# Performance work log

Hardware: AMD Instinct MI355X
Metric: run time of the kernel (lower is better)

## Reference

```python
import jax, jax.numpy as jnp
import numpy as np

B, N, M, C, H = 256, 4096, 64, 512, 4
IN, OUT = 64, 64
EPS = 1e-8

def setup_inputs():
    key = jax.random.key(0)
    ks = jax.random.split(key, 8)
    def w(k, shape, scale=0.05):
        return jax.random.normal(k, shape, dtype=jnp.float32) * scale
    return {
        "in_data": jax.random.normal(ks[0], (B, IN), dtype=jnp.float32),
        "memory": jax.random.normal(ks[1], (B, N, M), dtype=jnp.float32),
        "h0": jnp.zeros((B, C), jnp.float32),
        "c0": jnp.zeros((B, C), jnp.float32),
        "prev_weights": jnp.zeros((2 * H, B, N), jnp.float32),
        "prev_reads": jax.random.normal(ks[2], (H, B, M), dtype=jnp.float32),
        "W_ih": w(ks[3], (4 * C, IN + H * M)),
        "b_ih": jnp.zeros((4 * C,), jnp.float32),
        "W_hh": w(ks[4], (4 * C, C)),
        "b_hh": jnp.zeros((4 * C,), jnp.float32),
        "W_out": w(ks[5], (OUT, C + H * M)),
        "b_out": jnp.zeros((OUT,), jnp.float32),
        "W_addr": w(ks[6], (2 * H, M + 6, C)),
        "b_addr": jnp.zeros((2 * H, M + 6), jnp.float32),
        "W_ea": w(ks[7], (H, 2 * M, C)),
        "b_ea": jnp.zeros((H, 2 * M), jnp.float32),
    }


def reference(in_data, memory, h0, c0, prev_weights, prev_reads,
              W_ih, b_ih, W_hh, b_hh, W_out, b_out,
              W_addr, b_addr, W_ea, b_ea):
    # ---- controller: LSTMCell over [input, prev_reads...] ----
    x = jnp.concatenate([in_data] + [prev_reads[i] for i in range(H)], axis=-1)  # [B, IN+H*M]
    gates = x @ W_ih.T + b_ih + h0 @ W_hh.T + b_hh                               # [B, 4C]
    i_g, f_g, g_g, o_g = jnp.split(gates, 4, axis=-1)
    c = jax.nn.sigmoid(f_g) * c0 + jax.nn.sigmoid(i_g) * jnp.tanh(g_g)
    h = jax.nn.sigmoid(o_g) * jnp.tanh(c)

    # ---- heads: alternate read / write, sequential over memory ----
    mem = memory
    reads = []
    for hi in range(2 * H):
        p = c @ W_addr[hi].T + b_addr[hi]                     # [B, M+6]
        k = jnp.tanh(p[:, :M])                                # key
        beta = jax.nn.softplus(p[:, M:M + 1])                 # key strength
        gate = jax.nn.sigmoid(p[:, M + 1:M + 2])              # interpolation gate
        s = jax.nn.softmax(p[:, M + 2:M + 5], axis=-1)        # shift weights (3)
        gamma = 1.0 + jax.nn.softplus(p[:, M + 5:M + 6])      # sharpening
        # content addressing: cosine similarity against all memory rows
        dot = jnp.einsum('bnm,bm->bn', mem, k)                # [B, N]
        norms = jnp.linalg.norm(mem, axis=-1) * jnp.linalg.norm(k, axis=-1, keepdims=True)
        wc = jax.nn.softmax(beta * dot / (norms + EPS), axis=-1)
        # interpolation with previous weights
        wg = gate * wc + (1.0 - gate) * prev_weights[hi]
        # circular shift convolution (shifts -1, 0, +1)
        ws = (s[:, 0:1] * jnp.roll(wg, 1, axis=-1)
              + s[:, 1:2] * wg
              + s[:, 2:3] * jnp.roll(wg, -1, axis=-1))
        # sharpening
        wp = ws ** gamma
        w = wp / (jnp.sum(wp, axis=-1, keepdims=True) + EPS)
        if hi % 2 == 0:  # read head
            reads.append(jnp.einsum('bn,bnm->bm', w, mem))
        else:            # write head: erase then add
            ea = c @ W_ea[hi // 2].T + b_ea[hi // 2]          # [B, 2M]
            e = jax.nn.sigmoid(ea[:, :M])
            a = jnp.tanh(ea[:, M:])
            mem = mem * (1.0 - w[:, :, None] * e[:, None, :]) + w[:, :, None] * a[:, None, :]

    # ---- output layer over [h, reads...] ----
    state = jnp.concatenate([h] + reads, axis=-1)             # [B, C+H*M]
    return jax.nn.sigmoid(state @ W_out.T + b_out)            # [B, OUT]
```

## Files before the change

### kernel.cpp

```cpp
#include <hip/hip_runtime.h>
#include <math.h>

#define EPSF 1e-8f
#define PLANE ((size_t)256 * 4096)

__device__ __forceinline__ float sigf(float x) { return 1.0f / (1.0f + expf(-x)); }
__device__ __forceinline__ float softplusf(float x) { return x > 20.0f ? x : log1pf(expf(x)); }
__device__ __forceinline__ float dot4(float4 a, float4 b) {
  return a.x * b.x + a.y * b.y + a.z * b.z + a.w * b.w;
}
__device__ __forceinline__ unsigned short f2bf(float x) {
  unsigned int u = __float_as_uint(x);
  unsigned int r = (u + 0x7FFF + ((u >> 16) & 1)) >> 16;
  return (unsigned short)r;
}
__device__ __forceinline__ float bf2f(unsigned int lo16) {
  return __uint_as_float(lo16 << 16);
}

__device__ __forceinline__ float gather_x(const float* __restrict__ in_data,
                                          const float* __restrict__ prev_reads,
                                          const float* __restrict__ h0,
                                          int row, int k) {
  if (k < 64) return in_data[row * 64 + k];
// ... 86 lines not shown
      acc[0][0] += a0 * w0; acc[0][1] += a0 * w1; acc[0][2] += a0 * w2; acc[0][3] += a0 * w3;
      acc[1][0] += a1 * w0; acc[1][1] += a1 * w1; acc[1][2] += a1 * w2; acc[1][3] += a1 * w3;
    }
    __syncthreads();
  }
  for (int i = 0; i < 2; i++)
    for (int j = 0; j < 4; j++) {
      int col = col0 + tx * 4 + j;
      if (col < 1072) {
        float bias = col < 560 ? b_addr[col] : b_ea[col - 560];
        p_raw[(size_t)(row0 + ty * 2 + i) * 1072 + col] = acc[i][j] + bias;
      }
    }
}

__global__ void head_params_kernel(const float* __restrict__ p_raw,
    float* __restrict__ kvec, float* __restrict__ knorm,
    float* __restrict__ betav, float* __restrict__ gatev,
    float* __restrict__ sv, float* __restrict__ gammav,
    float* __restrict__ evec, float* __restrict__ avec) {
  int hi = blockIdx.x, b = blockIdx.y, t = threadIdx.x;
  const float* p = p_raw + (size_t)b * 1072 + hi * 70;
  if (t < 64) {
    float kvv = tanhf(p[t]);
    kvec[((size_t)hi * 256 + b) * 64 + t] = kvv;
    float s = kvv * kvv;
    for (int m = 1; m < 64; m <<= 1) s += __shfl_xor(s, m);
    if (t == 0) {
      int hb = hi * 256 + b;
      knorm[hb] = sqrtf(s);
      betav[hb] = softplusf(p[64]);
      gatev[hb] = sigf(p[65]);
      float a0 = p[66], a1 = p[67], a2 = p[68];
      float mm = fmaxf(a0, fmaxf(a1, a2));
      float e0 = expf(a0 - mm), e1 = expf(a1 - mm), e2 = expf(a2 - mm);
      float es = e0 + e1 + e2;
      sv[hb * 3 + 0] = e0 / es; sv[hb * 3 + 1] = e1 / es; sv[hb * 3 + 2] = e2 / es;
      gammav[hb] = 1.0f + softplusf(p[69]);
    }
  } else if ((hi & 1) && hi < 7) {
    int wj = hi >> 1, t2 = t - 64;
    const float* ea = p_raw + (size_t)b * 1072 + 560 + wj * 128;
    evec[((size_t)wj * 256 + b) * 64 + t2] = sigf(ea[t2]);
    avec[((size_t)wj * 256 + b) * 64 + t2] = tanhf(ea[64 + t2]);
  }
}

__global__ void combo_kernel(const float* __restrict__ kvec,
                             const float* __restrict__ evec,
                             const float* __restrict__ avec,
                             float* __restrict__ combo, float* __restrict__ scal) {
  int b = blockIdx.x, m = threadIdx.x;
  size_t bm = (size_t)b * 64 + m;
  float k0 = kvec[0 * 16384 + bm], k1 = kvec[1 * 16384 + bm];
  float k2 = kvec[2 * 16384 + bm], k3 = kvec[3 * 16384 + bm];
  float k4 = kvec[4 * 16384 + bm], k5 = kvec[5 * 16384 + bm];
  float k6 = kvec[6 * 16384 + bm];
  float e1 = evec[0 * 16384 + bm], a1 = avec[0 * 16384 + bm];
  float e3 = evec[1 * 16384 + bm], a3 = avec[1 * 16384 + bm];
  float e5 = evec[2 * 16384 + bm], a5 = avec[2 * 16384 + bm];
  combo[0 * 16384 + bm] = k0;  combo[1 * 16384 + bm] = k1;
  combo[2 * 16384 + bm] = k2;  combo[3 * 16384 + bm] = e1 * k2;
  combo[4 * 16384 + bm] = k3;  combo[5 * 16384 + bm] = e1 * k3;
  combo[6 * 16384 + bm] = a1;  combo[7 * 16384 + bm] = e1 * a1;
  combo[8 * 16384 + bm] = e1;  combo[9 * 16384 + bm] = e1 * e1;
  combo[10 * 16384 + bm] = k4; combo[11 * 16384 + bm] = k5;
  combo[12 * 16384 + bm] = k6; combo[13 * 16384 + bm] = e5 * k6;
  combo[14 * 16384 + bm] = a5; combo[15 * 16384 + bm] = e5 * a5;
  combo[16 * 16384 + bm] = e5; combo[17 * 16384 + bm] = e5 * e5;
  combo[18 * 16384 + bm] = e3; combo[19 * 16384 + bm] = a3;
  float s0 = a1 * k2, s1 = a1 * k3, s2 = a1 * a1, s3 = a5 * k6, s4 = a5 * a5;
#pragma unroll
  for (int d = 1; d < 64; d <<= 1) {
    s0 += __shfl_xor(s0, d); s1 += __shfl_xor(s1, d); s2 += __shfl_xor(s2, d);
    s3 += __shfl_xor(s3, d); s4 += __shfl_xor(s4, d);
  }
  if (m == 0) {
    scal[b * 8 + 0] = s0; scal[b * 8 + 1] = s1; scal[b * 8 + 2] = s2;
    scal[b * 8 + 3] = s3; scal[b * 8 + 4] = s4;
  }
}

#define LDC(j, q) (*(const float4*)(cb + (size_t)(j) * 16384 + (q) * 4))

__global__ __launch_bounds__(256) void dotpass1_kernel(
    const float* __restrict__ mem, const float* __restrict__ combo,
    const float* __restrict__ knorm, const float* __restrict__ betav,
    const float* __restrict__ scal, float* __restrict__ P1,
    unsigned short* __restrict__ mem_bf) {
  extern __shared__ float4 tile[];
  const int NN = 4096;
  int b = blockIdx.y, n0 = blockIdx.x * 256, tid = threadIdx.x;
  const float4* m4 = (const float4*)mem + ((size_t)b * NN + n0) * 16;
  ushort4* mb4 = (ushort4*)mem_bf + ((size_t)b * NN + n0) * 16;
#pragma unroll
  for (int i = 0; i < 16; i++) {
    int L = tid + i * 256, r = L >> 4, q = L & 15;
    float4 v = m4[L];
    tile[r * 16 + (q ^ (r & 15))] = v;
    ushort4 o;
    o.x = f2bf(v.x); o.y = f2bf(v.y); o.z = f2bf(v.z); o.w = f2bf(v.w);
    mb4[L] = o;
  }
  __syncthreads();
  const float* cb = combo + (size_t)b * 64;
  float d0=0,d1=0,d2=0,d3=0,d4=0,d5=0,d6=0,d7=0,s0=0,s1=0,s2=0;
#pragma unroll
  for (int q = 0; q < 16; q++) {
    float4 v = tile[tid * 16 + (q ^ (tid & 15))];
    float4 sq = make_float4(v.x*v.x, v.y*v.y, v.z*v.z, v.w*v.w);
    d0 += dot4(v, LDC(0, q)); d1 += dot4(v, LDC(1, q));
    d2 += dot4(v, LDC(2, q)); d3 += dot4(v, LDC(3, q));
    d4 += dot4(v, LDC(4, q)); d5 += dot4(v, LDC(5, q));
    d6 += dot4(v, LDC(6, q)); d7 += dot4(v, LDC(7, q));
    s0 += sq.x + sq.y + sq.z + sq.w;
    s1 += dot4(sq, LDC(8, q)); s2 += dot4(sq, LDC(9, q));
  }
  float kn0 = knorm[0 * 256 + b], be0 = betav[0 * 256 + b];
  float kn1 = knorm[1 * 256 + b], be1 = betav[1 * 256 + b];
  float cak2 = scal[b * 8 + 0], cak3 = scal[b * 8 + 1], caa = scal[b * 8 + 2];
  float rn = sqrtf(s0);
  size_t o = (size_t)b * NN + n0 + tid;
  P1[0*PLANE+o] = be0 * d0 / (rn * kn0 + EPSF);
  P1[1*PLANE+o] = be1 * d1 / (rn * kn1 + EPSF);
  P1[2*PLANE+o] = d2; P1[3*PLANE+o] = d3 - cak2;
  P1[4*PLANE+o] = d4; P1[5*PLANE+o] = d5 - cak3;
  P1[6*PLANE+o] = s0; P1[7*PLANE+o] = s1 - d6; P1[8*PLANE+o] = s2 - 2.f*d7 + caa;
}

__global__ __launch_bounds__(256) void dotpass2_kernel(
    const unsigned short* __restrict__ mem_bf, const float* __restrict__ combo,
    const float* __restrict__ w_all, const float* __restrict__ knorm,
    const float* __restrict__ betav, const float* __restrict__ scal,
    float* __restrict__ P2) {
  __shared__ uint4 tileb[2048];
  const int NN = 4096;
  int b = blockIdx.y, n0 = blockIdx.x * 256, tid = threadIdx.x;
  size_t bo = (size_t)b * NN;
  const uint4* mb = (const uint4*)mem_bf + (bo + n0) * 8;
#pragma unroll
  for (int i = 0; i < 8; i++) {
    int G = tid + i * 256, r = G >> 3, g = G & 7;
    tileb[r * 8 + (g ^ (r & 7))] = mb[G];
  }
  __syncthreads();
  const float* cb = combo + (size_t)b * 64;
  float u1 = w_all[1 * PLANE + bo + n0 + tid];
  float u3 = w_all[3 * PLANE + bo + n0 + tid];
  float t0=0,t1=0,t2=0,t3=0,t4=0,t5=0,r0=0,r1=0,r2=0;
#pragma unroll
  for (int g = 0; g < 8; g++) {
    uint4 uv = tileb[tid * 8 + (g ^ (tid & 7))];
#pragma unroll
    for (int h = 0; h < 2; h++) {
      unsigned int pa = h ? uv.z : uv.x;
      unsigned int pb = h ? uv.w : uv.y;
      float4 v;
      v.x = bf2f(pa & 0xFFFFu); v.y = bf2f(pa >> 16);
      v.z = bf2f(pb & 0xFFFFu); v.w = bf2f(pb >> 16);
      int q = g * 2 + h;
      float4 e1 = LDC(8, q), aa1 = LDC(6, q), e3 = LDC(18, q), aa3 = LDC(19, q);
      float4 m1, m2;
      m1.x = v.x * (1.f - u1 * e1.x) + u1 * aa1.x;
      m1.y = v.y * (1.f - u1 * e1.y) + u1 * aa1.y;
      m1.z = v.z * (1.f - u1 * e1.z) + u1 * aa1.z;
      m1.w = v.w * (1.f - u1 * e1.w) + u1 * aa1.w;
      m2.x = m1.x * (1.f - u3 * e3.x) + u3 * aa3.x;
      m2.y = m1.y * (1.f - u3 * e3.y) + u3 * aa3.y;
      m2.z = m1.z * (1.f - u3 * e3.z) + u3 * aa3.z;
      m2.w = m1.w * (1.f - u3 * e3.w) + u3 * aa3.w;
      float4 sq = make_float4(m2.x*m2.x, m2.y*m2.y, m2.z*m2.z, m2.w*m2.w);
      t0 += dot4(m2, LDC(10, q)); t1 += dot4(m2, LDC(11, q));
      t2 += dot4(m2, LDC(12, q)); t3 += dot4(m2, LDC(13, q));
      t4 += dot4(m2, LDC(14, q)); t5 += dot4(m2, LDC(15, q));
      r0 += sq.x + sq.y + sq.z + sq.w;
      r1 += dot4(sq, LDC(16, q)); r2 += dot4(sq, LDC(17, q));
    }
  }
  float kn4 = knorm[4 * 256 + b], be4 = betav[4 * 256 + b];
  float kn5 = knorm[5 * 256 + b], be5 = betav[5 * 256 + b];
  float cak6 = scal[b * 8 + 3], caa6 = scal[b * 8 + 4];
  float rn = sqrtf(r0);
  size_t o = bo + n0 + tid;
  P2[0*PLANE+o] = be4 * t0 / (rn * kn4 + EPSF);
  P2[1*PLANE+o] = be5 * t1 / (rn * kn5 + EPSF);
  P2[2*PLANE+o] = t2; P2[3*PLANE+o] = t3 - cak6;
  P2[4*PLANE+o] = r0; P2[5*PLANE+o] = r1 - t4; P2[6*PLANE+o] = r2 - 2.f*t5 + caa6;
}

__global__ __launch_bounds__(256) void readpass_kernel(
    const unsigned short* __restrict__ mem_bf, const float* __restrict__ w_all,
    const float* __restrict__ evec, const float* __restrict__ avec,
    float* __restrict__ reads) {
  const int NN = 4096;
  int b = blockIdx.y, n0 = blockIdx.x * 256, tid = threadIdx.x;
  int wv = tid >> 6, lane = tid & 63, q = lane & 15, rl = lane >> 4;
  size_t bo = (size_t)b * NN;
  float4 e1 = *(const float4*)(evec + 0 * 16384 + b * 64 + q * 4);
  float4 a1 = *(const float4*)(avec + 0 * 16384 + b * 64 + q * 4);
  float4 e3 = *(const float4*)(evec + 1 * 16384 + b * 64 + q * 4);
  float4 a3 = *(const float4*)(avec + 1 * 16384 + b * 64 + q * 4);
  float4 e5 = *(const float4*)(evec + 2 * 16384 + b * 64 + q * 4);
  float4 a5 = *(const float4*)(avec + 2 * 16384 + b * 64 + q * 4);
  const float* w0r = w_all + 0 * PLANE + bo;
  const float* w1r = w_all + 1 * PLANE + bo;
  const float* w2r = w_all + 2 * PLANE + bo;
  const float* w3r = w_all + 3 * PLANE + bo;
  const float* w4r = w_all + 4 * PLANE + bo;
  const float* w5r = w_all + 5 * PLANE + bo;
  const float* w6r = w_all + 6 * PLANE + bo;
  __shared__ float sred[4][4][16][4];
  const ushort4* mb = (const ushort4*)mem_bf;
  float A[4][4] = {{0,0,0,0},{0,0,0,0},{0,0,0,0},{0,0,0,0}};
#pragma unroll 4
  for (int t = 0; t < 16; t++) {
    int nl = wv * 64 + t * 4 + rl, n = n0 + nl;
    ushort4 uv = mb[(bo + n0 + (size_t)nl) * 16 + q];
    float vx = bf2f(uv.x), vy = bf2f(uv.y), vz = bf2f(uv.z), vw = bf2f(uv.w);
    float w0v = w0r[n], u1 = w1r[n], w2v = w2r[n], u3 = w3r[n];
    float w4v = w4r[n], u5 = w5r[n], w6v = w6r[n];
    A[0][0] += w0v * vx; A[0][1] += w0v * vy; A[0][2] += w0v * vz; A[0][3] += w0v * vw;
    float m1x = vx * (1.f - u1 * e1.x) + u1 * a1.x;
    float m1y = vy * (1.f - u1 * e1.y) + u1 * a1.y;
    float m1z = vz * (1.f - u1 * e1.z) + u1 * a1.z;
    float m1w = vw * (1.f - u1 * e1.w) + u1 * a1.w;
    A[1][0] += w2v * m1x; A[1][1] += w2v * m1y; A[1][2] += w2v * m1z; A[1][3] += w2v * m1w;
    float m2x = m1x * (1.f - u3 * e3.x) + u3 * a3.x;
    float m2y = m1y * (1.f - u3 * e3.y) + u3 * a3.y;
    float m2z = m1z * (1.f - u3 * e3.z) + u3 * a3.z;
    float m2w = m1w * (1.f - u3 * e3.w) + u3 * a3.w;
    A[2][0] += w4v * m2x; A[2][1] += w4v * m2y; A[2][2] += w4v * m2z; A[2][3] += w4v * m2w;
    float m3x = m2x * (1.f - u5 * e5.x) + u5 * a5.x;
    float m3y = m2y * (1.f - u5 * e5.y) + u5 * a5.y;
    float m3z = m2z * (1.f - u5 * e5.z) + u5 * a5.z;
    float m3w = m2w * (1.f - u5 * e5.w) + u5 * a5.w;
    A[3][0] += w6v * m3x; A[3][1] += w6v * m3y; A[3][2] += w6v * m3z; A[3][3] += w6v * m3w;
  }
#pragma unroll
  for (int j = 0; j < 4; j++)
#pragma unroll
    for (int cmp = 0; cmp < 4; cmp++) {
      float x = A[j][cmp];
#pragma unroll
      for (int m = 16; m < 64; m <<= 1) x += __shfl_xor(x, m);
      A[j][cmp] = x;
    }
  if (rl == 0)
#pragma unroll
    for (int j = 0; j < 4; j++) {
      sred[j][wv][q][0] = A[j][0]; sred[j][wv][q][1] = A[j][1];
      sred[j][wv][q][2] = A[j][2]; sred[j][wv][q][3] = A[j][3];
    }
  __syncthreads();
  if (tid < 64) {
    int qq = tid >> 2, cc = tid & 3;
#pragma unroll
    for (int j = 0; j < 4; j++) {
      float s = sred[j][0][qq][cc] + sred[j][1][qq][cc] + sred[j][2][qq][cc] + sred[j][3][qq][cc];
      atomicAdd(&reads[j * 16384 + b * 64 + qq * 4 + cc], s);
    }
  }
}

template<int ND, int NE>
__global__ __launch_bounds__(256) void chain_kernel(
    const float* __restrict__ P, const float* __restrict__ uplane,
    const float* __restrict__ knorm, const float* __restrict__ betav,
    const float* __restrict__ gatev, const float* __restrict__ sv,
    const float* __restrict__ gammav, const float* __restrict__ prev_w,
    float* __restrict__ w_all, int head_base) {
  const int NN = 4096, BB = 256;
  int slot = blockIdx.x, b = blockIdx.y;
  int head = head_base + slot;
  size_t bo = (size_t)b * NN;
  __shared__ float wg[4096];
  __shared__ float redm[4], reds[4], reds2[4];
  int tid = threadIdx.x;
  int lane = tid & 63, wv = tid >> 6;
  int hb = head * BB + b;
  float kn = knorm[hb], be = betav[hb], ga = gatev[hb], gm = gammav[hb];
  float s0 = sv[hb * 3 + 0], s1 = sv[hb * 3 + 1], s2 = sv[hb * 3 + 2];
  const float* SC  = P + (size_t)slot * PLANE;
  const float* Da  = P + (size_t)(ND + 2 * (slot - ND)) * PLANE;
  const float* Dbc = Da + PLANE;
  const float* S0p = P + (size_t)(ND + 2 * NE) * PLANE;
  const float* T1p = S0p + PLANE;
  const float* T2p = T1p + PLANE;

  float sc[16];
  float mx = -1e30f;
#pragma unroll
  for (int i = 0; i < 16; i++) {
    int n = tid + i * 256;
    float scv;
    if (slot < ND) {
      scv = SC[bo + n];
    } else {
      float u = uplane[bo + n];
      float d = Da[bo + n] - u * Dbc[bo + n];
      float nn2 = S0p[bo + n] - 2.f * u * T1p[bo + n] + u * u * T2p[bo + n];
      nn2 = fmaxf(nn2, 0.f);
      scv = be * d / (sqrtf(nn2) * kn + EPSF);
    }
    sc[i] = scv;
    mx = fmaxf(mx, scv);
  }
  for (int m = 1; m < 64; m <<= 1) mx = fmaxf(mx, __shfl_xor(mx, m));
  if (lane == 0) redm[wv] = mx;
  __syncthreads();
  mx = fmaxf(fmaxf(redm[0], redm[1]), fmaxf(redm[2], redm[3]));
  float sum = 0.f;
#pragma unroll
  for (int i = 0; i < 16; i++) { sc[i] = expf(sc[i] - mx); sum += sc[i]; }
  for (int m = 1; m < 64; m <<= 1) sum += __shfl_xor(sum, m);
  if (lane == 0) reds[wv] = sum;
  __syncthreads();
  sum = reds[0] + reds[1] + reds[2] + reds[3];
  float inv = 1.0f / sum;
  const float* pw = prev_w + (size_t)head * BB * NN + bo;
#pragma unroll
  for (int i = 0; i < 16; i++) {
    int n = tid + i * 256;
    wg[n] = ga * (sc[i] * inv) + (1.f - ga) * pw[n];
  }
  __syncthreads();
  float wp[16];
  float sum2 = 0.f;
#pragma unroll
  for (int i = 0; i < 16; i++) {
    int n = tid + i * 256;
    float wsv = s0 * wg[(n + NN - 1) & (NN - 1)] + s1 * wg[n] + s2 * wg[(n + 1) & (NN - 1)];
    wp[i] = powf(wsv, gm);
    sum2 += wp[i];
  }
  for (int m = 1; m < 64; m <<= 1) sum2 += __shfl_xor(sum2, m);
  if (lane == 0) reds2[wv] = sum2;
  __syncthreads();
  sum2 = reds2[0] + reds2[1] + reds2[2] + reds2[3];
  float invs = 1.0f / (sum2 + EPSF);
  float* wo = w_all + (size_t)head * BB * NN + bo;
#pragma unroll
  for (int i = 0; i < 16; i++) wo[tid + i * 256] = wp[i] * invs;
}

__global__ __launch_bounds__(256) void gemm_out_kernel(
    const float* __restrict__ h, const float* __restrict__ reads,
    const float* __restrict__ W_out, const float* __restrict__ b_out,
    float* __restrict__ out) {
  __shared__ float As[16][33];
  __shared__ float Ws[16][65];
  int tid = threadIdx.x, tx = tid & 15, ty = tid >> 4;
  int row0 = blockIdx.y * 32;
  float acc[2][4] = {{0,0,0,0},{0,0,0,0}};
  for (int k0 = 0; k0 < 768; k0 += 16) {
    for (int i = tid; i < 32 * 16; i += 256) {
      int rr = i >> 4, cc = i & 15;
      int row = row0 + rr, k = k0 + cc;
// ... 41 lines not shown
  const float* b_out   = (const float*)d_in[11];
  const float* W_addr  = (const float*)d_in[12];
  const float* b_addr  = (const float*)d_in[13];
  const float* W_ea    = (const float*)d_in[14];
  const float* b_ea    = (const float*)d_in[15];
  float* out = (float*)d_out;
  (void)in_sizes; (void)n_in; (void)out_size; (void)ws_size;

  float* ws = (float*)d_ws;
  size_t off = 0;
  auto alloc = [&](size_t n) { float* p = ws + off; off += (n + 63) & ~(size_t)63; return p; };
  float* gates  = alloc(256 * 2048);
  float* cbuf   = alloc(256 * 512);
  float* hbuf   = alloc(256 * 512);
  float* p_raw  = alloc(256 * 1072);
  float* kvec   = alloc(8 * 256 * 64);
  float* knorm  = alloc(8 * 256);
  float* betav  = alloc(8 * 256);
  float* gatev  = alloc(8 * 256);
  float* sv     = alloc(8 * 256 * 3);
  float* gammav = alloc(8 * 256);
  float* evec   = alloc(3 * 256 * 64);
  float* avec   = alloc(3 * 256 * 64);
  float* combo  = alloc(20 * 256 * 64);
  float* scal   = alloc(256 * 8);
  float* P1     = alloc(9 * PLANE);
  float* P2     = alloc(7 * PLANE);
  float* w_all  = alloc(7 * PLANE);
  float* reads  = alloc(4 * 256 * 64);
  unsigned short* mem_bf = (unsigned short*)alloc(33554432);

  hipMemsetAsync(reads, 0, 4 * 256 * 64 * sizeof(float), stream);

  gemm_gates_kernel<<<dim3(32, 8), 256, 0, stream>>>(in_data, prev_r, h0, W_ih, W_hh, b_ih, b_hh, gates);
  lstm_elem_kernel<<<(256 * 512 + 255) / 256, 256, 0, stream>>>(gates, c0, cbuf, hbuf);
  gemm_heads_kernel<<<dim3(17, 8), 256, 0, stream>>>(cbuf, W_addr, W_ea, b_addr, b_ea, p_raw);
  head_params_kernel<<<dim3(8, 256), 128, 0, stream>>>(p_raw, kvec, knorm, betav, gatev, sv, gammav, evec, avec);
  combo_kernel<<<256, 64, 0, stream>>>(kvec, evec, avec, combo, scal);

  dim3 pgrid(16, 256);
  dotpass1_kernel<<<pgrid, 256, 65536, stream>>>(memory, combo, knorm, betav, scal, P1, mem_bf);
  chain_kernel<2, 2><<<dim3(4, 256), 256, 0, stream>>>(
      P1, w_all + 1 * PLANE, knorm, betav, gatev, sv, gammav, prev_w, w_all, 0);
  dotpass2_kernel<<<pgrid, 256, 0, stream>>>(mem_bf, combo, w_all, knorm, betav, scal, P2);
  chain_kernel<2, 1><<<dim3(3, 256), 256, 0, stream>>>(
      P2, w_all + 5 * PLANE, knorm, betav, gatev, sv, gammav, prev_w, w_all, 4);
  readpass_kernel<<<pgrid, 256, 0, stream>>>(mem_bf, w_all, evec, avec, reads);

  gemm_out_kernel<<<dim3(1, 8), 256, 0, stream>>>(hbuf, reads, W_out, b_out, out);
}
```

Measured before the change: 921.9 us.

## Fuse memory passes and chains into one per-batch mega kernel with fp16 planes

```diff
diff --git a/kernel.cpp b/kernel.cpp
--- a/kernel.cpp
+++ b/kernel.cpp
@@ -1,8 +1,11 @@
 #include <hip/hip_runtime.h>
+#include <hip/hip_fp16.h>
 #include <math.h>
 
 #define EPSF 1e-8f
-#define PLANE ((size_t)256 * 4096)
+#define NN 4096
+#define BB 256
+#define PH ((size_t)BB * NN)
 
 __device__ __forceinline__ float sigf(float x) { return 1.0f / (1.0f + expf(-x)); }
 __device__ __forceinline__ float softplusf(float x) { return x > 20.0f ? x : log1pf(expf(x)); }
@@ -124,62 +127,49 @@
     }
 }
 
-__global__ void head_params_kernel(const float* __restrict__ p_raw,
-    float* __restrict__ kvec, float* __restrict__ knorm,
-    float* __restrict__ betav, float* __restrict__ gatev,
-    float* __restrict__ sv, float* __restrict__ gammav,
-    float* __restrict__ evec, float* __restrict__ avec) {
-  int hi = blockIdx.x, b = blockIdx.y, t = threadIdx.x;
-  const float* p = p_raw + (size_t)b * 1072 + hi * 70;
-  if (t < 64) {
-    float kvv = tanhf(p[t]);
-    kvec[((size_t)hi * 256 + b) * 64 + t] = kvv;
-    float s = kvv * kvv;
-    for (int m = 1; m < 64; m <<= 1) s += __shfl_xor(s, m);
-    if (t == 0) {
-      int hb = hi * 256 + b;
+__global__ void params_kernel(const float* __restrict__ p_raw,
+    float* __restrict__ knorm, float* __restrict__ betav,
+    float* __restrict__ gatev, float* __restrict__ sv,
+    float* __restrict__ gammav, float* __restrict__ combo,
+    float* __restrict__ scal) {
+  int b = blockIdx.x, m = threadIdx.x;
+  const float* p = p_raw + (size_t)b * 1072;
+  float kv[7];
+#pragma unroll
+  for (int hi = 0; hi < 7; hi++) {
+    float k = tanhf(p[hi * 70 + m]);
+    kv[hi] = k;
+    float s = k * k;
+#pragma unroll
+    for (int d = 1; d < 64; d <<= 1) s += __shfl_xor(s, d);
+    if (m == 0) {
+      int hb = hi * BB + b;
       knorm[hb] = sqrtf(s);
-      betav[hb] = softplusf(p[64]);
-      gatev[hb] = sigf(p[65]);
-      float a0 = p[66], a1 = p[67], a2 = p[68];
+      betav[hb] = softplusf(p[hi * 70 + 64]);
+      gatev[hb] = sigf(p[hi * 70 + 65]);
+      float a0 = p[hi * 70 + 66], a1 = p[hi * 70 + 67], a2 = p[hi * 70 + 68];
       float mm = fmaxf(a0, fmaxf(a1, a2));
       float e0 = expf(a0 - mm), e1 = expf(a1 - mm), e2 = expf(a2 - mm);
       float es = e0 + e1 + e2;
       sv[hb * 3 + 0] = e0 / es; sv[hb * 3 + 1] = e1 / es; sv[hb * 3 + 2] = e2 / es;
-      gammav[hb] = 1.0f + softplusf(p[69]);
-    }
-  } else if ((hi & 1) && hi < 7) {
-    int wj = hi >> 1, t2 = t - 64;
-    const float* ea = p_raw + (size_t)b * 1072 + 560 + wj * 128;
-    evec[((size_t)wj * 256 + b) * 64 + t2] = sigf(ea[t2]);
-    avec[((size_t)wj * 256 + b) * 64 + t2] = tanhf(ea[64 + t2]);
-  }
-}
-
-__global__ void combo_kernel(const float* __restrict__ kvec,
-                             const float* __restrict__ evec,
-                             const float* __restrict__ avec,
-                             float* __restrict__ combo, float* __restrict__ scal) {
-  int b = blockIdx.x, m = threadIdx.x;
+      gammav[hb] = 1.0f + softplusf(p[hi * 70 + 69]);
+    }
+  }
+  float e1 = sigf(p[560 + 0 * 128 + m]),  a1v = tanhf(p[560 + 0 * 128 + 64 + m]);
+  float e3 = sigf(p[560 + 1 * 128 + m]),  a3v = tanhf(p[560 + 1 * 128 + 64 + m]);
+  float e5 = sigf(p[560 + 2 * 128 + m]),  a5v = tanhf(p[560 + 2 * 128 + 64 + m]);
   size_t bm = (size_t)b * 64 + m;
-  float k0 = kvec[0 * 16384 + bm], k1 = kvec[1 * 16384 + bm];
-  float k2 = kvec[2 * 16384 + bm], k3 = kvec[3 * 16384 + bm];
-  float k4 = kvec[4 * 16384 + bm], k5 = kvec[5 * 16384 + bm];
-  float k6 = kvec[6 * 16384 + bm];
-  float e1 = evec[0 * 16384 + bm], a1 = avec[0 * 16384 + bm];
-  float e3 = evec[1 * 16384 + bm], a3 = avec[1 * 16384 + bm];
-  float e5 = evec[2 * 16384 + bm], a5 = avec[2 * 16384 + bm];
-  combo[0 * 16384 + bm] = k0;  combo[1 * 16384 + bm] = k1;
-  combo[2 * 16384 + bm] = k2;  combo[3 * 16384 + bm] = e1 * k2;
-  combo[4 * 16384 + bm] = k3;  combo[5 * 16384 + bm] = e1 * k3;
-  combo[6 * 16384 + bm] = a1;  combo[7 * 16384 + bm] = e1 * a1;
-  combo[8 * 16384 + bm] = e1;  combo[9 * 16384 + bm] = e1 * e1;
-  combo[10 * 16384 + bm] = k4; combo[11 * 16384 + bm] = k5;
-  combo[12 * 16384 + bm] = k6; combo[13 * 16384 + bm] = e5 * k6;
-  combo[14 * 16384 + bm] = a5; combo[15 * 16384 + bm] = e5 * a5;
-  combo[16 * 16384 + bm] = e5; combo[17 * 16384 + bm] = e5 * e5;
-  combo[18 * 16384 + bm] = e3; combo[19 * 16384 + bm] = a3;
-  float s0 = a1 * k2, s1 = a1 * k3, s2 = a1 * a1, s3 = a5 * k6, s4 = a5 * a5;
+  combo[0 * 16384 + bm] = kv[0];  combo[1 * 16384 + bm] = kv[1];
+  combo[2 * 16384 + bm] = kv[2];  combo[3 * 16384 + bm] = e1 * kv[2];
+  combo[4 * 16384 + bm] = kv[3];  combo[5 * 16384 + bm] = e1 * kv[3];
+  combo[6 * 16384 + bm] = a1v;    combo[7 * 16384 + bm] = e1 * a1v;
+  combo[8 * 16384 + bm] = e1;     combo[9 * 16384 + bm] = e1 * e1;
+  combo[10 * 16384 + bm] = kv[4]; combo[11 * 16384 + bm] = kv[5];
+  combo[12 * 16384 + bm] = kv[6]; combo[13 * 16384 + bm] = e5 * kv[6];
+  combo[14 * 16384 + bm] = a5v;   combo[15 * 16384 + bm] = e5 * a5v;
+  combo[16 * 16384 + bm] = e5;    combo[17 * 16384 + bm] = e5 * e5;
+  combo[18 * 16384 + bm] = e3;    combo[19 * 16384 + bm] = a3v;
+  float s0 = a1v * kv[2], s1 = a1v * kv[3], s2 = a1v * a1v, s3 = a5v * kv[6], s4 = a5v * a5v;
 #pragma unroll
   for (int d = 1; d < 64; d <<= 1) {
     s0 += __shfl_xor(s0, d); s1 += __shfl_xor(s1, d); s2 += __shfl_xor(s2, d);
@@ -191,266 +181,323 @@
   }
 }
 
-#define LDC(j, q) (*(const float4*)(cb + (size_t)(j) * 16384 + (q) * 4))
-
-__global__ __launch_bounds__(256) void dotpass1_kernel(
-    const float* __restrict__ mem, const float* __restrict__ combo,
-    const float* __restrict__ knorm, const float* __restrict__ betav,
-    const float* __restrict__ scal, float* __restrict__ P1,
-    unsigned short* __restrict__ mem_bf) {
-  extern __shared__ float4 tile[];
-  const int NN = 4096;
-  int b = blockIdx.y, n0 = blockIdx.x * 256, tid = threadIdx.x;
-  const float4* m4 = (const float4*)mem + ((size_t)b * NN + n0) * 16;
-  ushort4* mb4 = (ushort4*)mem_bf + ((size_t)b * NN + n0) * 16;
-#pragma unroll
-  for (int i = 0; i < 16; i++) {
-    int L = tid + i * 256, r = L >> 4, q = L & 15;
-    float4 v = m4[L];
-    tile[r * 16 + (q ^ (r & 15))] = v;
-    ushort4 o;
-    o.x = f2bf(v.x); o.y = f2bf(v.y); o.z = f2bf(v.z); o.w = f2bf(v.w);
-    mb4[L] = o;
-  }
-  __syncthreads();
-  const float* cb = combo + (size_t)b * 64;
-  float d0=0,d1=0,d2=0,d3=0,d4=0,d5=0,d6=0,d7=0,s0=0,s1=0,s2=0;
-#pragma unroll
-  for (int q = 0; q < 16; q++) {
-    float4 v = tile[tid * 16 + (q ^ (tid & 15))];
-    float4 sq = make_float4(v.x*v.x, v.y*v.y, v.z*v.z, v.w*v.w);
-    d0 += dot4(v, LDC(0, q)); d1 += dot4(v, LDC(1, q));
-    d2 += dot4(v, LDC(2, q)); d3 += dot4(v, LDC(3, q));
-    d4 += dot4(v, LDC(4, q)); d5 += dot4(v, LDC(5, q));
-    d6 += dot4(v, LDC(6, q)); d7 += dot4(v, LDC(7, q));
-    s0 += sq.x + sq.y + sq.z + sq.w;
-    s1 += dot4(sq, LDC(8, q)); s2 += dot4(sq, LDC(9, q));
-  }
-  float kn0 = knorm[0 * 256 + b], be0 = betav[0 * 256 + b];
-  float kn1 = knorm[1 * 256 + b], be1 = betav[1 * 256 + b];
-  float cak2 = scal[b * 8 + 0], cak3 = scal[b * 8 + 1], caa = scal[b * 8 + 2];
-  float rn = sqrtf(s0);
-  size_t o = (size_t)b * NN + n0 + tid;
-  P1[0*PLANE+o] = be0 * d0 / (rn * kn0 + EPSF);
-  P1[1*PLANE+o] = be1 * d1 / (rn * kn1 + EPSF);
-  P1[2*PLANE+o] = d2; P1[3*PLANE+o] = d3 - cak2;
-  P1[4*PLANE+o] = d4; P1[5*PLANE+o] = d5 - cak3;
-  P1[6*PLANE+o] = s0; P1[7*PLANE+o] = s1 - d6; P1[8*PLANE+o] = s2 - 2.f*d7 + caa;
-}
-
-__global__ __launch_bounds__(256) void dotpass2_kernel(
-    const unsigned short* __restrict__ mem_bf, const float* __restrict__ combo,
-    const float* __restrict__ w_all, const float* __restrict__ knorm,
-    const float* __restrict__ betav, const float* __restrict__ scal,
-    float* __restrict__ P2) {
-  __shared__ uint4 tileb[2048];
-  const int NN = 4096;
-  int b = blockIdx.y, n0 = blockIdx.x * 256, tid = threadIdx.x;
-  size_t bo = (size_t)b * NN;
-  const uint4* mb = (const uint4*)mem_bf + (bo + n0) * 8;
-#pragma unroll
-  for (int i = 0; i < 8; i++) {
-    int G = tid + i * 256, r = G >> 3, g = G & 7;
-    tileb[r * 8 + (g ^ (r & 7))] = mb[G];
-  }
-  __syncthreads();
-  const float* cb = combo + (size_t)b * 64;
-  float u1 = w_all[1 * PLANE + bo + n0 + tid];
-  float u3 = w_all[3 * PLANE + bo + n0 + tid];
-  float t0=0,t1=0,t2=0,t3=0,t4=0,t5=0,r0=0,r1=0,r2=0;
-#pragma unroll
-  for (int g = 0; g < 8; g++) {
-    uint4 uv = tileb[tid * 8 + (g ^ (tid & 7))];
-#pragma unroll
-    for (int h = 0; h < 2; h++) {
-      unsigned int pa = h ? uv.z : uv.x;
-      unsigned int pb = h ? uv.w : uv.y;
-      float4 v;
-      v.x = bf2f(pa & 0xFFFFu); v.y = bf2f(pa >> 16);
-      v.z = bf2f(pb & 0xFFFFu); v.w = bf2f(pb >> 16);
-      int q = g * 2 + h;
-      float4 e1 = LDC(8, q), aa1 = LDC(6, q), e3 = LDC(18, q), aa3 = LDC(19, q);
-      float4 m1, m2;
-      m1.x = v.x * (1.f - u1 * e1.x) + u1 * aa1.x;
-      m1.y = v.y * (1.f - u1 * e1.y) + u1 * aa1.y;
-      m1.z = v.z * (1.f - u1 * e1.z) + u1 * aa1.z;
-      m1.w = v.w * (1.f - u1 * e1.w) + u1 * aa1.w;
-      m2.x = m1.x * (1.f - u3 * e3.x) + u3 * aa3.x;
-      m2.y = m1.y * (1.f - u3 * e3.y) + u3 * aa3.y;
-      m2.z = m1.z * (1.f - u3 * e3.z) + u3 * aa3.z;
-      m2.w = m1.w * (1.f - u3 * e3.w) + u3 * aa3.w;
-      float4 sq = make_float4(m2.x*m2.x, m2.y*m2.y, m2.z*m2.z, m2.w*m2.w);
-      t0 += dot4(m2, LDC(10, q)); t1 += dot4(m2, LDC(11, q));
-      t2 += dot4(m2, LDC(12, q)); t3 += dot4(m2, LDC(13, q));
-      t4 += dot4(m2, LDC(14, q)); t5 += dot4(m2, LDC(15, q));
-      r0 += sq.x + sq.y + sq.z + sq.w;
-      r1 += dot4(sq, LDC(16, q)); r2 += dot4(sq, LDC(17, q));
-    }
-  }
-  float kn4 = knorm[4 * 256 + b], be4 = betav[4 * 256 + b];
-  float kn5 = knorm[5 * 256 + b], be5 = betav[5 * 256 + b];
-  float cak6 = scal[b * 8 + 3], caa6 = scal[b * 8 + 4];
-  float rn = sqrtf(r0);
-  size_t o = bo + n0 + tid;
-  P2[0*PLANE+o] = be4 * t0 / (rn * kn4 + EPSF);
-  P2[1*PLANE+o] = be5 * t1 / (rn * kn5 + EPSF);
-  P2[2*PLANE+o] = t2; P2[3*PLANE+o] = t3 - cak6;
-  P2[4*PLANE+o] = r0; P2[5*PLANE+o] = r1 - t4; P2[6*PLANE+o] = r2 - 2.f*t5 + caa6;
-}
-
-__global__ __launch_bounds__(256) void readpass_kernel(
-    const unsigned short* __restrict__ mem_bf, const float* __restrict__ w_all,
-    const float* __restrict__ evec, const float* __restrict__ avec,
-    float* __restrict__ reads) {
-  const int NN = 4096;
-  int b = blockIdx.y, n0 = blockIdx.x * 256, tid = threadIdx.x;
-  int wv = tid >> 6, lane = tid & 63, q = lane & 15, rl = lane >> 4;
-  size_t bo = (size_t)b * NN;
-  float4 e1 = *(const float4*)(evec + 0 * 16384 + b * 64 + q * 4);
-  float4 a1 = *(const float4*)(avec + 0 * 16384 + b * 64 + q * 4);
-  float4 e3 = *(const float4*)(evec + 1 * 16384 + b * 64 + q * 4);
-  float4 a3 = *(const float4*)(avec + 1 * 16384 + b * 64 + q * 4);
-  float4 e5 = *(const float4*)(evec + 2 * 16384 + b * 64 + q * 4);
-  float4 a5 = *(const float4*)(avec + 2 * 16384 + b * 64 + q * 4);
-  const float* w0r = w_all + 0 * PLANE + bo;
-  const float* w1r = w_all + 1 * PLANE + bo;
-  const float* w2r = w_all + 2 * PLANE + bo;
-  const float* w3r = w_all + 3 * PLANE + bo;
-  const float* w4r = w_all + 4 * PLANE + bo;
-  const float* w5r = w_all + 5 * PLANE + bo;
-  const float* w6r = w_all + 6 * PLANE + bo;
-  __shared__ float sred[4][4][16][4];
-  const ushort4* mb = (const ushort4*)mem_bf;
-  float A[4][4] = {{0,0,0,0},{0,0,0,0},{0,0,0,0},{0,0,0,0}};
-#pragma unroll 4
-  for (int t = 0; t < 16; t++) {
-    int nl = wv * 64 + t * 4 + rl, n = n0 + nl;
-    ushort4 uv = mb[(bo + n0 + (size_t)nl) * 16 + q];
-    float vx = bf2f(uv.x), vy = bf2f(uv.y), vz = bf2f(uv.z), vw = bf2f(uv.w);
-    float w0v = w0r[n], u1 = w1r[n], w2v = w2r[n], u3 = w3r[n];
-    float w4v = w4r[n], u5 = w5r[n], w6v = w6r[n];
-    A[0][0] += w0v * vx; A[0][1] += w0v * vy; A[0][2] += w0v * vz; A[0][3] += w0v * vw;
-    float m1x = vx * (1.f - u1 * e1.x) + u1 * a1.x;
-    float m1y = vy * (1.f - u1 * e1.y) + u1 * a1.y;
-    float m1z = vz * (1.f - u1 * e1.z) + u1 * a1.z;
-    float m1w = vw * (1.f - u1 * e1.w) + u1 * a1.w;
-    A[1][0] += w2v * m1x; A[1][1] += w2v * m1y; A[1][2] += w2v * m1z; A[1][3] += w2v * m1w;
-    float m2x = m1x * (1.f - u3 * e3.x) + u3 * a3.x;
-    float m2y = m1y * (1.f - u3 * e3.y) + u3 * a3.y;
-    float m2z = m1z * (1.f - u3 * e3.z) + u3 * a3.z;
-    float m2w = m1w * (1.f - u3 * e3.w) + u3 * a3.w;
-    A[2][0] += w4v * m2x; A[2][1] += w4v * m2y; A[2][2] += w4v * m2z; A[2][3] += w4v * m2w;
-    float m3x = m2x * (1.f - u5 * e5.x) + u5 * a5.x;
-    float m3y = m2y * (1.f - u5 * e5.y) + u5 * a5.y;
-    float m3z = m2z * (1.f - u5 * e5.z) + u5 * a5.z;
-    float m3w = m2w * (1.f - u5 * e5.w) + u5 * a5.w;
-    A[3][0] += w6v * m3x; A[3][1] += w6v * m3y; A[3][2] += w6v * m3z; A[3][3] += w6v * m3w;
-  }
-#pragma unroll
-  for (int j = 0; j < 4; j++)
-#pragma unroll
-    for (int cmp = 0; cmp < 4; cmp++) {
-      float x = A[j][cmp];
-#pragma unroll
-      for (int m = 16; m < 64; m <<= 1) x += __shfl_xor(x, m);
-      A[j][cmp] = x;
-    }
-  if (rl == 0)
-#pragma unroll
-    for (int j = 0; j < 4; j++) {
-      sred[j][wv][q][0] = A[j][0]; sred[j][wv][q][1] = A[j][1];
-      sred[j][wv][q][2] = A[j][2]; sred[j][wv][q][3] = A[j][3];
-    }
-  __syncthreads();
-  if (tid < 64) {
-    int qq = tid >> 2, cc = tid & 3;
-#pragma unroll
-    for (int j = 0; j < 4; j++) {
-      float s = sred[j][0][qq][cc] + sred[j][1][qq][cc] + sred[j][2][qq][cc] + sred[j][3][qq][cc];
-      atomicAdd(&reads[j * 16384 + b * 64 + qq * 4 + cc], s);
-    }
-  }
-}
-
-template<int ND, int NE>
-__global__ __launch_bounds__(256) void chain_kernel(
-    const float* __restrict__ P, const float* __restrict__ uplane,
+#define CL(j, q) (*(const float4*)(cb + (j) * 64 + (q) * 4))
+
+__device__ void chain_dev(int tid, int b, int head,
+    const __half* __restrict__ SC, const __half* __restrict__ Da,
+    const __half* __restrict__ Dbc, const __half* __restrict__ S0p,
+    const __half* __restrict__ T1p, const __half* __restrict__ T2p,
+    const __half* w_h, int u_head, __half* w_out,
+    float* wg, float* red,
     const float* __restrict__ knorm, const float* __restrict__ betav,
     const float* __restrict__ gatev, const float* __restrict__ sv,
-    const float* __restrict__ gammav, const float* __restrict__ prev_w,
-    float* __restrict__ w_all, int head_base) {
-  const int NN = 4096, BB = 256;
-  int slot = blockIdx.x, b = blockIdx.y;
-  int head = head_base + slot;
-  size_t bo = (size_t)b * NN;
-  __shared__ float wg[4096];
-  __shared__ float redm[4], reds[4], reds2[4];
-  int tid = threadIdx.x;
+    const float* __restrict__ gammav, const float* __restrict__ prev_w) {
   int lane = tid & 63, wv = tid >> 6;
   int hb = head * BB + b;
   float kn = knorm[hb], be = betav[hb], ga = gatev[hb], gm = gammav[hb];
   float s0 = sv[hb * 3 + 0], s1 = sv[hb * 3 + 1], s2 = sv[hb * 3 + 2];
-  const float* SC  = P + (size_t)slot * PLANE;
-  const float* Da  = P + (size_t)(ND + 2 * (slot - ND)) * PLANE;
-  const float* Dbc = Da + PLANE;
-  const float* S0p = P + (size_t)(ND + 2 * NE) * PLANE;
-  const float* T1p = S0p + PLANE;
-  const float* T2p = T1p + PLANE;
-
-  float sc[16];
+  size_t bo = (size_t)b * NN;
+  const float* pw = prev_w + (size_t)head * PH + bo;
+  float sc[8];
   float mx = -1e30f;
 #pragma unroll
-  for (int i = 0; i < 16; i++) {
-    int n = tid + i * 256;
+  for (int i = 0; i < 8; i++) {
+    int n = tid + i * 512;
     float scv;
-    if (slot < ND) {
-      scv = SC[bo + n];
+    if (SC != nullptr) {
+      scv = __half2float(SC[bo + n]);
     } else {
-      float u = uplane[bo + n];
-      float d = Da[bo + n] - u * Dbc[bo + n];
-      float nn2 = S0p[bo + n] - 2.f * u * T1p[bo + n] + u * u * T2p[bo + n];
+      float u = __half2float(w_h[u_head * NN + n]);
+      float d = __half2float(Da[bo + n]) - u * __half2float(Dbc[bo + n]);
+      float nn2 = __half2float(S0p[bo + n]) - 2.f * u * __half2float(T1p[bo + n])
+                + u * u * __half2float(T2p[bo + n]);
       nn2 = fmaxf(nn2, 0.f);
       scv = be * d / (sqrtf(nn2) * kn + EPSF);
     }
-    sc[i] = scv;
-    mx = fmaxf(mx, scv);
-  }
+    sc[i] = scv; mx = fmaxf(mx, scv);
+  }
+#pragma unroll
   for (int m = 1; m < 64; m <<= 1) mx = fmaxf(mx, __shfl_xor(mx, m));
-  if (lane == 0) redm[wv] = mx;
+  if (lane == 0) red[wv] = mx;
   __syncthreads();
-  mx = fmaxf(fmaxf(redm[0], redm[1]), fmaxf(redm[2], redm[3]));
+  mx = red[0];
+#pragma unroll
+  for (int w = 1; w < 8; w++) mx = fmaxf(mx, red[w]);
   float sum = 0.f;
 #pragma unroll
-  for (int i = 0; i < 16; i++) { sc[i] = expf(sc[i] - mx); sum += sc[i]; }
+  for (int i = 0; i < 8; i++) { sc[i] = expf(sc[i] - mx); sum += sc[i]; }
+#pragma unroll
   for (int m = 1; m < 64; m <<= 1) sum += __shfl_xor(sum, m);
-  if (lane == 0) reds[wv] = sum;
+  if (lane == 0) red[8 + wv] = sum;
   __syncthreads();
-  sum = reds[0] + reds[1] + reds[2] + reds[3];
+  sum = 0.f;
+#pragma unroll
+  for (int w = 0; w < 8; w++) sum += red[8 + w];
   float inv = 1.0f / sum;
-  const float* pw = prev_w + (size_t)head * BB * NN + bo;
-#pragma unroll
-  for (int i = 0; i < 16; i++) {
-    int n = tid + i * 256;
+#pragma unroll
+  for (int i = 0; i < 8; i++) {
+    int n = tid + i * 512;
     wg[n] = ga * (sc[i] * inv) + (1.f - ga) * pw[n];
   }
   __syncthreads();
-  float wp[16];
+  float wp[8];
   float sum2 = 0.f;
 #pragma unroll
-  for (int i = 0; i < 16; i++) {
-    int n = tid + i * 256;
+  for (int i = 0; i < 8; i++) {
+    int n = tid + i * 512;
     float wsv = s0 * wg[(n + NN - 1) & (NN - 1)] + s1 * wg[n] + s2 * wg[(n + 1) & (NN - 1)];
     wp[i] = powf(wsv, gm);
     sum2 += wp[i];
   }
+#pragma unroll
   for (int m = 1; m < 64; m <<= 1) sum2 += __shfl_xor(sum2, m);
-  if (lane == 0) reds2[wv] = sum2;
+  if (lane == 0) red[16 + wv] = sum2;
   __syncthreads();
-  sum2 = reds2[0] + reds2[1] + reds2[2] + reds2[3];
+  sum2 = 0.f;
+#pragma unroll
+  for (int w = 0; w < 8; w++) sum2 += red[16 + w];
   float invs = 1.0f / (sum2 + EPSF);
-  float* wo = w_all + (size_t)head * BB * NN + bo;
-#pragma unroll
-  for (int i = 0; i < 16; i++) wo[tid + i * 256] = wp[i] * invs;
+#pragma unroll
+  for (int i = 0; i < 8; i++) {
+    int n = tid + i * 512;
+    w_out[n] = __float2half(wp[i] * invs);
+  }
+  __syncthreads();
+}
+
+__global__ __launch_bounds__(512, 2) void mega_kernel(
+    const float* __restrict__ mem, const float* __restrict__ combo,
+    const float* __restrict__ scal, const float* __restrict__ knorm,
+    const float* __restrict__ betav, const float* __restrict__ gatev,
+    const float* __restrict__ sv, const float* __restrict__ gammav,
+    const float* __restrict__ prev_w, unsigned short* __restrict__ mem_bf,
+    __half* __restrict__ P, float* __restrict__ reads) {
+  extern __shared__ char smem[];
+  __half* w_h   = (__half*)smem;
+  float*  cb    = (float*)(smem + 57344);
+  float*  scr   = (float*)(smem + 62464);
+  char*   un    = smem + 84992;
+  float4* tile32 = (float4*)un;
+  uint4*  tileb  = (uint4*)un;
+  float*  wg     = (float*)un;
+
+  int b = blockIdx.x, tid = threadIdx.x;
+  size_t bo = (size_t)b * NN;
+
+  for (int i = tid; i < 1280; i += 512) {
+    int j = i >> 6, m = i & 63;
+    cb[i] = combo[(size_t)j * 16384 + b * 64 + m];
+  }
+  __syncthreads();
+
+  {
+    float kn0 = knorm[0 * BB + b], be0 = betav[0 * BB + b];
+    float kn1 = knorm[1 * BB + b], be1 = betav[1 * BB + b];
+    float cak2 = scal[b * 8 + 0], cak3 = scal[b * 8 + 1], caa1 = scal[b * 8 + 2];
+    const float4* m4 = (const float4*)mem + bo * 16;
+    ushort4* mb4 = (ushort4*)mem_bf + bo * 16;
+    for (int c = 0; c < 16; c++) {
+      int gbase = c * 4096;
+#pragma unroll
+      for (int i = 0; i < 8; i++) {
+        int G = tid + i * 512;
+        float4 v = m4[gbase + G];
+        int r = G >> 4, q = G & 15;
+        tile32[r * 16 + (q ^ (r & 15))] = v;
+        ushort4 o;
+        o.x = f2bf(v.x); o.y = f2bf(v.y); o.z = f2bf(v.z); o.w = f2bf(v.w);
+        mb4[gbase + G] = o;
+      }
+      __syncthreads();
+      int r = tid & 255, qb = (tid >> 8) * 8;
+      float a[11];
+#pragma unroll
+      for (int k = 0; k < 11; k++) a[k] = 0.f;
+#pragma unroll
+      for (int j = 0; j < 8; j++) {
+        int q = qb + j;
+        float4 v = tile32[r * 16 + (q ^ (r & 15))];
+        float4 sq = make_float4(v.x * v.x, v.y * v.y, v.z * v.z, v.w * v.w);
+        a[0] += dot4(v, CL(0, q)); a[1] += dot4(v, CL(1, q));
+        a[2] += dot4(v, CL(2, q)); a[3] += dot4(v, CL(3, q));
+        a[4] += dot4(v, CL(4, q)); a[5] += dot4(v, CL(5, q));
+        a[6] += dot4(v, CL(6, q)); a[7] += dot4(v, CL(7, q));
+        a[8] += sq.x + sq.y + sq.z + sq.w;
+        a[9] += dot4(sq, CL(8, q)); a[10] += dot4(sq, CL(9, q));
+      }
+#pragma unroll
+      for (int k = 0; k < 11; k++) scr[tid * 11 + k] = a[k];
+      __syncthreads();
+      if (tid < 256) {
+#pragma unroll
+        for (int k = 0; k < 11; k++) a[k] = scr[tid * 11 + k] + scr[(tid + 256) * 11 + k];
+        int n = c * 256 + tid;
+        float rn = sqrtf(a[8]);
+        P[0 * PH + bo + n] = __float2half(be0 * a[0] / (rn * kn0 + EPSF));
+        P[1 * PH + bo + n] = __float2half(be1 * a[1] / (rn * kn1 + EPSF));
+        P[2 * PH + bo + n] = __float2half(a[2]);
+        P[3 * PH + bo + n] = __float2half(a[3] - cak2);
+        P[4 * PH + bo + n] = __float2half(a[4]);
+        P[5 * PH + bo + n] = __float2half(a[5] - cak3);
+        P[6 * PH + bo + n] = __float2half(a[8]);
+        P[7 * PH + bo + n] = __float2half(a[9] - a[6]);
+        P[8 * PH + bo + n] = __float2half(a[10] - 2.f * a[7] + caa1);
+      }
+      __syncthreads();
+    }
+  }
+
+  chain_dev(tid, b, 0, P + 0 * PH, nullptr, nullptr, nullptr, nullptr, nullptr,
+            w_h, 0, w_h + 0 * NN, wg, scr, knorm, betav, gatev, sv, gammav, prev_w);
+  chain_dev(tid, b, 1, P + 1 * PH, nullptr, nullptr, nullptr, nullptr, nullptr,
+            w_h, 0, w_h + 1 * NN, wg, scr, knorm, betav, gatev, sv, gammav, prev_w);
+  chain_dev(tid, b, 2, nullptr, P + 2 * PH, P + 3 * PH, P + 6 * PH, P + 7 * PH, P + 8 * PH,
+            w_h, 1, w_h + 2 * NN, wg, scr, knorm, betav, gatev, sv, gammav, prev_w);
+  chain_dev(tid, b, 3, nullptr, P + 4 * PH, P + 5 * PH, P + 6 * PH, P + 7 * PH, P + 8 * PH,
+            w_h, 1, w_h + 3 * NN, wg, scr, knorm, betav, gatev, sv, gammav, prev_w);
+
+  {
+    float kn4 = knorm[4 * BB + b], be4 = betav[4 * BB + b];
+    float kn5 = knorm[5 * BB + b], be5 = betav[5 * BB + b];
+    float cak6 = scal[b * 8 + 3], caa5 = scal[b * 8 + 4];
+    const uint4* mb16 = (const uint4*)mem_bf + bo * 8;
+    for (int c = 0; c < 16; c++) {
+      int gbase = c * 2048;
+#pragma unroll
+      for (int i = 0; i < 4; i++) {
+        int G = tid + i * 512;
+        uint4 u = mb16[gbase + G];
+        int r = G >> 3, g = G & 7;
+        tileb[r * 8 + (g ^ (r & 7))] = u;
+      }
+      __syncthreads();
+      int r = tid & 255, gb2 = (tid >> 8) * 4;
+      float u1 = __half2float(w_h[1 * NN + c * 256 + r]);
+      float u3 = __half2float(w_h[3 * NN + c * 256 + r]);
+      float t[9];
+#pragma unroll
+      for (int k = 0; k < 9; k++) t[k] = 0.f;
+#pragma unroll
+      for (int j = 0; j < 4; j++) {
+        int g = gb2 + j;
+        uint4 uv = tileb[r * 8 + (g ^ (r & 7))];
+#pragma unroll
+        for (int h = 0; h < 2; h++) {
+          unsigned int pa = h ? uv.z : uv.x;
+          unsigned int pb = h ? uv.w : uv.y;
+          float4 v;
+          v.x = bf2f(pa & 0xFFFFu); v.y = bf2f(pa >> 16);
+          v.z = bf2f(pb & 0xFFFFu); v.w = bf2f(pb >> 16);
+          int q = g * 2 + h;
+          float4 e1v = CL(8, q), a1v = CL(6, q), e3v = CL(18, q), a3v = CL(19, q);
+          float4 m1, m2;
+          m1.x = v.x * (1.f - u1 * e1v.x) + u1 * a1v.x;
+          m1.y = v.y * (1.f - u1 * e1v.y) + u1 * a1v.y;
+          m1.z = v.z * (1.f - u1 * e1v.z) + u1 * a1v.z;
+          m1.w = v.w * (1.f - u1 * e1v.w) + u1 * a1v.w;
+          m2.x = m1.x * (1.f - u3 * e3v.x) + u3 * a3v.x;
+          m2.y = m1.y * (1.f - u3 * e3v.y) + u3 * a3v.y;
+          m2.z = m1.z * (1.f - u3 * e3v.z) + u3 * a3v.z;
+          m2.w = m1.w * (1.f - u3 * e3v.w) + u3 * a3v.w;
+          float4 sq = make_float4(m2.x * m2.x, m2.y * m2.y, m2.z * m2.z, m2.w * m2.w);
+          t[0] += dot4(m2, CL(10, q)); t[1] += dot4(m2, CL(11, q));
+          t[2] += dot4(m2, CL(12, q)); t[3] += dot4(m2, CL(13, q));
+          t[4] += dot4(m2, CL(14, q)); t[5] += dot4(m2, CL(15, q));
+          t[6] += sq.x + sq.y + sq.z + sq.w;
+          t[7] += dot4(sq, CL(16, q)); t[8] += dot4(sq, CL(17, q));
+        }
+      }
+#pragma unroll
+      for (int k = 0; k < 9; k++) scr[tid * 9 + k] = t[k];
+      __syncthreads();
+      if (tid < 256) {
+#pragma unroll
+        for (int k = 0; k < 9; k++) t[k] = scr[tid * 9 + k] + scr[(tid + 256) * 9 + k];
+        int n = c * 256 + tid;
+        float rn = sqrtf(t[6]);
+        P[0 * PH + bo + n] = __float2half(be4 * t[0] / (rn * kn4 + EPSF));
+        P[1 * PH + bo + n] = __float2half(be5 * t[1] / (rn * kn5 + EPSF));
+        P[2 * PH + bo + n] = __float2half(t[2]);
+        P[3 * PH + bo + n] = __float2half(t[3] - cak6);
+        P[4 * PH + bo + n] = __float2half(t[6]);
+        P[5 * PH + bo + n] = __float2half(t[7] - t[4]);
+        P[6 * PH + bo + n] = __float2half(t[8] - 2.f * t[5] + caa5);
+      }
+      __syncthreads();
+    }
+  }
+
+  chain_dev(tid, b, 4, P + 0 * PH, nullptr, nullptr, nullptr, nullptr, nullptr,
+            w_h, 0, w_h + 4 * NN, wg, scr, knorm, betav, gatev, sv, gammav, prev_w);
+  chain_dev(tid, b, 5, P + 1 * PH, nullptr, nullptr, nullptr, nullptr, nullptr,
+            w_h, 0, w_h + 5 * NN, wg, scr, knorm, betav, gatev, sv, gammav, prev_w);
+  chain_dev(tid, b, 6, nullptr, P + 2 * PH, P + 3 * PH, P + 4 * PH, P + 5 * PH, P + 6 * PH,
+            w_h, 5, w_h + 6 * NN, wg, scr, knorm, betav, gatev, sv, gammav, prev_w);
+
+  {
+    int wv = tid >> 6, lane = tid & 63, q = lane & 15, rl = lane >> 4;
+    float4 e1v = CL(8, q), a1v = CL(6, q), e3v = CL(18, q), a3v = CL(19, q);
+    float4 e5v = CL(16, q), a5v = CL(14, q);
+    const ushort4* mbr = (const ushort4*)mem_bf + bo * 16;
+    float A[4][4];
+#pragma unroll
+    for (int j = 0; j < 4; j++)
+#pragma unroll
+      for (int cmp = 0; cmp < 4; cmp++) A[j][cmp] = 0.f;
+#pragma unroll 4
+    for (int t = 0; t < 128; t++) {
+      int n = t * 32 + wv * 4 + rl;
+      ushort4 uv = mbr[(size_t)n * 16 + q];
+      float vx = bf2f(uv.x), vy = bf2f(uv.y), vz = bf2f(uv.z), vw = bf2f(uv.w);
+      float w0v = __half2float(w_h[0 * NN + n]);
+      float u1  = __half2float(w_h[1 * NN + n]);
+      float w2v = __half2float(w_h[2 * NN + n]);
+      float u3  = __half2float(w_h[3 * NN + n]);
+      float w4v = __half2float(w_h[4 * NN + n]);
+      float u5  = __half2float(w_h[5 * NN + n]);
+      float w6v = __half2float(w_h[6 * NN + n]);
+      A[0][0] += w0v * vx; A[0][1] += w0v * vy; A[0][2] += w0v * vz; A[0][3] += w0v * vw;
+      float m1x = vx * (1.f - u1 * e1v.x) + u1 * a1v.x;
+      float m1y = vy * (1.f - u1 * e1v.y) + u1 * a1v.y;
+      float m1z = vz * (1.f - u1 * e1v.z) + u1 * a1v.z;
+      float m1w = vw * (1.f - u1 * e1v.w) + u1 * a1v.w;
+      A[1][0] += w2v * m1x; A[1][1] += w2v * m1y; A[1][2] += w2v * m1z; A[1][3] += w2v * m1w;
+      float m2x = m1x * (1.f - u3 * e3v.x) + u3 * a3v.x;
+      float m2y = m1y * (1.f - u3 * e3v.y) + u3 * a3v.y;
+      float m2z = m1z * (1.f - u3 * e3v.z) + u3 * a3v.z;
+      float m2w = m1w * (1.f - u3 * e3v.w) + u3 * a3v.w;
+      A[2][0] += w4v * m2x; A[2][1] += w4v * m2y; A[2][2] += w4v * m2z; A[2][3] += w4v * m2w;
+      float m3x = m2x * (1.f - u5 * e5v.x) + u5 * a5v.x;
+      float m3y = m2y * (1.f - u5 * e5v.y) + u5 * a5v.y;
+      float m3z = m2z * (1.f - u5 * e5v.z) + u5 * a5v.z;
+      float m3w = m2w * (1.f - u5 * e5v.w) + u5 * a5v.w;
+      A[3][0] += w6v * m3x; A[3][1] += w6v * m3y; A[3][2] += w6v * m3z; A[3][3] += w6v * m3w;
+    }
+#pragma unroll
+    for (int j = 0; j < 4; j++)
+#pragma unroll
+      for (int cmp = 0; cmp < 4; cmp++) {
+        float x = A[j][cmp];
+        x += __shfl_xor(x, 16);
+        x += __shfl_xor(x, 32);
+        A[j][cmp] = x;
+      }
+    float* sred = scr;
+    if (rl == 0)
+#pragma unroll
+      for (int j = 0; j < 4; j++)
+#pragma unroll
+        for (int cmp = 0; cmp < 4; cmp++)
+          sred[((j * 8 + wv) * 16 + q) * 4 + cmp] = A[j][cmp];
+    __syncthreads();
+    if (tid < 256) {
+      int j = tid >> 6, qq = (tid >> 2) & 15, cc = tid & 3;
+      float s = 0.f;
+#pragma unroll
+      for (int w = 0; w < 8; w++) s += sred[((j * 8 + w) * 16 + qq) * 4 + cc];
+      reads[(size_t)j * 16384 + b * 64 + qq * 4 + cc] = s;
+    }
+  }
 }
 
 __global__ __launch_bounds__(256) void gemm_out_kernel(
@@ -522,38 +569,29 @@
   float* cbuf   = alloc(256 * 512);
   float* hbuf   = alloc(256 * 512);
   float* p_raw  = alloc(256 * 1072);
-  float* kvec   = alloc(8 * 256 * 64);
   float* knorm  = alloc(8 * 256);
   float* betav  = alloc(8 * 256);
   float* gatev  = alloc(8 * 256);
   float* sv     = alloc(8 * 256 * 3);
   float* gammav = alloc(8 * 256);
-  float* evec   = alloc(3 * 256 * 64);
-  float* avec   = alloc(3 * 256 * 64);
-  float* combo  = alloc(20 * 256 * 64);
+  float* combo  = alloc(20 * 16384);
   float* scal   = alloc(256 * 8);
-  float* P1     = alloc(9 * PLANE);
-  float* P2     = alloc(7 * PLANE);
-  float* w_all  = alloc(7 * PLANE);
-  float* reads  = alloc(4 * 256 * 64);
+  __half* P     = (__half*)alloc(9 * PH / 2);
+  float* reads  = alloc(4 * 16384);
   unsigned short* mem_bf = (unsigned short*)alloc(33554432);
 
-  hipMemsetAsync(reads, 0, 4 * 256 * 64 * sizeof(float), stream);
+  static bool attr_set = false;
+  if (!attr_set) {
+    hipFuncSetAttribute((const void*)mega_kernel,
+                        hipFuncAttributeMaxDynamicSharedMemorySize, 150528);
+    attr_set = true;
+  }
 
   gemm_gates_kernel<<<dim3(32, 8), 256, 0, stream>>>(in_data, prev_r, h0, W_ih, W_hh, b_ih, b_hh, gates);
   lstm_elem_kernel<<<(256 * 512 + 255) / 256, 256, 0, stream>>>(gates, c0, cbuf, hbuf);
   gemm_heads_kernel<<<dim3(17, 8), 256, 0, stream>>>(cbuf, W_addr, W_ea, b_addr, b_ea, p_raw);
-  head_params_kernel<<<dim3(8, 256), 128, 0, stream>>>(p_raw, kvec, knorm, betav, gatev, sv, gammav, evec, avec);
-  combo_kernel<<<256, 64, 0, stream>>>(kvec, evec, avec, combo, scal);
-
-  dim3 pgrid(16, 256);
-  dotpass1_kernel<<<pgrid, 256, 65536, stream>>>(memory, combo, knorm, betav, scal, P1, mem_bf);
-  chain_kernel<2, 2><<<dim3(4, 256), 256, 0, stream>>>(
-      P1, w_all + 1 * PLANE, knorm, betav, gatev, sv, gammav, prev_w, w_all, 0);
-  dotpass2_kernel<<<pgrid, 256, 0, stream>>>(mem_bf, combo, w_all, knorm, betav, scal, P2);
-  chain_kernel<2, 1><<<dim3(3, 256), 256, 0, stream>>>(
-      P2, w_all + 5 * PLANE, knorm, betav, gatev, sv, gammav, prev_w, w_all, 4);
-  readpass_kernel<<<pgrid, 256, 0, stream>>>(mem_bf, w_all, evec, avec, reads);
-
+  params_kernel<<<256, 64, 0, stream>>>(p_raw, knorm, betav, gatev, sv, gammav, combo, scal);
+  mega_kernel<<<256, 512, 150528, stream>>>(memory, combo, scal, knorm, betav, gatev,
+                                            sv, gammav, prev_w, mem_bf, P, reads);
   gemm_out_kernel<<<dim3(1, 8), 256, 0, stream>>>(hbuf, reads, W_out, b_out, out);
 }
```

Measured after the change: 899.1 us. -2.5%, faster.
